# Performance work log

Measured on AMD Instinct MI355X. Metric: run time of the kernel, lower is better.

The kernel has to match this reference:

```python
import jax, jax.numpy as jnp
import numpy as np

N_NODES = 32768
N_EDGES = 524288
NODE_DIM, POS_DIM, EDGE_DIM = 44, 8, 1
HID, OUT, LAYERS, HEADS = 128, 128, 3, 4
DK = HID // HEADS
LN_EPS = 1e-5


def _linear_w(key, fan_in, fan_out):
    return (jax.random.normal(key, (fan_in, fan_out), jnp.float32) / np.sqrt(fan_in)).astype(jnp.float32)


def _ln(x, g, b):
    m = jnp.mean(x, axis=-1, keepdims=True)
    v = jnp.var(x, axis=-1, keepdims=True)
    return (x - m) * jax.lax.rsqrt(v + LN_EPS) * g + b


def setup_inputs() -> dict:
    key = jax.random.key(0)
    ks = jax.random.split(key, 16)
    inp = {
        'feats': jax.random.normal(ks[0], (N_NODES, NODE_DIM), jnp.float32),
        'lap_pos_enc': jax.random.normal(ks[1], (N_NODES, POS_DIM), jnp.float32),
        'edge_feats': jax.random.normal(ks[2], (N_EDGES, EDGE_DIM), jnp.float32),
        'src': jax.random.randint(ks[3], (N_EDGES,), 0, N_NODES, jnp.int32),
        'dst': jax.random.randint(ks[4], (N_EDGES,), 0, N_NODES, jnp.int32),
        # input projections
        'W_node': _linear_w(ks[5], NODE_DIM, HID), 'b_node': jnp.zeros((HID,), jnp.float32),
        'W_pos': _linear_w(ks[6], POS_DIM, HID), 'b_pos': jnp.zeros((HID,), jnp.float32),
        'W_edge': _linear_w(ks[7], EDGE_DIM, HID), 'b_edge': jnp.zeros((HID,), jnp.float32),
    }
    # per-layer stacked params (all layers are HID->HID since OUT==HID)
    def stack(k, fi, fo):
        kk = jax.random.split(k, LAYERS)
        return jnp.stack([_linear_w(kk[i], fi, fo) for i in range(LAYERS)])
    inp['Wq'] = stack(ks[8], HID, HID)
    inp['Wk'] = stack(ks[9], HID, HID)
    inp['Wv'] = stack(ks[10], HID, HID)
    inp['We'] = stack(ks[11], HID, HID)
    inp['W_lin'] = stack(ks[12], HID, HID)
    inp['b_lin'] = jnp.zeros((LAYERS, HID), jnp.float32)
    inp['g1'] = jnp.ones((LAYERS, HID), jnp.float32)
    inp['be1'] = jnp.zeros((LAYERS, HID), jnp.float32)
    inp['Wf1'] = stack(ks[13], HID, 2 * HID)
    inp['bf1'] = jnp.zeros((LAYERS, 2 * HID), jnp.float32)
    inp['Wf2'] = stack(ks[14], 2 * HID, HID)
    inp['bf2'] = jnp.zeros((LAYERS, HID), jnp.float32)
    inp['g2'] = jnp.ones((LAYERS, HID), jnp.float32)
    inp['be2'] = jnp.zeros((LAYERS, HID), jnp.float32)
    return inp


def reference(feats, lap_pos_enc, edge_feats,
              W_node, b_node, W_pos, b_pos, W_edge, b_edge,
              Wq, Wk, Wv, We, W_lin, b_lin, g1, be1,
              Wf1, bf1, Wf2, bf2, g2, be2, src, dst):
    n = feats.shape[0]
    inv_sqrt_dk = np.float32(1.0 / np.sqrt(DK))
    h = feats @ W_node + b_node + lap_pos_enc @ W_pos + b_pos      # [N, HID]
    e = edge_feats @ W_edge + b_edge                               # [E, HID] (shared across layers)
    for i in range(LAYERS):
        Q = (h @ Wq[i]).reshape(n, HEADS, DK)
        K = (h @ Wk[i]).reshape(n, HEADS, DK)
        V = (h @ Wv[i]).reshape(n, HEADS, DK)
        E = (e @ We[i]).reshape(-1, HEADS, DK)                     # [E, H, DK]
        # raw score [E, H, 1] broadcast against (1+E) -> [E, H, DK] (faithful to source)
        score = jnp.sum(K[src] * Q[dst], axis=-1, keepdims=True) * inv_sqrt_dk
        score = score * (1.0 + E)
        alpha = jnp.exp(score)                                      # [E, H, DK]
        Z = jnp.maximum(jax.ops.segment_sum(alpha, dst, num_segments=n), 1e-6)
        h_out = jax.ops.segment_sum(V[src] * alpha, dst, num_segments=n) / Z
        h_out = h_out.reshape(n, HEADS * DK)
        h = h + h_out @ W_lin[i] + b_lin[i]                        # residual + dropout(identity)
        h = _ln(h, g1[i], be1[i])
        h2 = jax.nn.relu(h @ Wf1[i] + bf1[i]) @ Wf2[i] + bf2[i]
        h = _ln(h + h2, g2[i], be2[i])
    # dgl.mean_nodes over a single graph -> [1, OUT]; readout LayerNorm is never applied in source
    return jnp.mean(h, axis=0, keepdims=True)
```

## Files before the change

kernel.cpp:

```cpp
#include <hip/hip_runtime.h>
#include <hip/hip_bf16.h>

#define N_NODES 32768
#define N_EDGES 524288
#define LN_EPS 1e-5f

typedef unsigned short ushort_t;
typedef __attribute__((ext_vector_type(8))) short short8v;
typedef __attribute__((ext_vector_type(4))) float float4v;

__device__ __forceinline__ float bf2f(ushort_t u) {
    return __uint_as_float(((unsigned int)u) << 16);
}
__device__ __forceinline__ ushort_t f2bf(float f) {
    unsigned int u = __float_as_uint(f);
    unsigned int r = (u + 0x7FFFu + ((u >> 16) & 1u)) >> 16;
    return (ushort_t)r;
}
__device__ __forceinline__ float lo16(unsigned int x) { return __uint_as_float(x << 16); }
__device__ __forceinline__ float hi16(unsigned int x) { return __uint_as_float(x & 0xFFFF0000u); }

#if __has_builtin(__builtin_amdgcn_exp2f)
#define EXP2(x) __builtin_amdgcn_exp2f(x)
#else
#define EXP2(x) exp2f(x)
#endif

#define OFF_WNODE 0
#define OFF_BNODE 5632
#define OFF_WPOS  5760
#define OFF_BPOS  6784
#define OFF_WEDGE 6912
#define OFF_BEDGE 7040
#define OFF_WQ    7168
#define OFF_WK    56320
#define OFF_WV    105472
#define OFF_WE    154624
#define OFF_WLIN  203776
#define OFF_BLIN  252928
#define OFF_G1    253312
#define OFF_BE1   253696
#define OFF_WF1   254080
#define OFF_BF1   352384
#define OFF_WF2   353152
#define OFF_BF2   451456
#define OFF_G2    451840
#define OFF_BE2   452224
#define CONV_TOTAL 452608

#define REC_QKV(i)  ((i) * 96)
#define REC_WLIN(i) (288 + (i) * 32)
#define REC_WF1(i)  (384 + (i) * 64)
#define REC_WF2(i)  (576 + (i) * 64)
#define REC_TOTAL   768

#define LDS_STRIDE 264
#define LDS_FSTRIDE 132

__global__ void detect_kernel(const unsigned int* __restrict__ wn, int* __restrict__ flag) {
    __shared__ int s[256];
    int t = threadIdx.x;
    int cnt = 0;
    for (int i = t; i < 2816; i += 256) {
        unsigned int b = (wn[i] >> 8) & 0x7F;
        cnt += (b >= 0x3A && b <= 0x40) ? 1 : 0;
    }
    s[t] = cnt;
    __syncthreads();
    for (int off = 128; off > 0; off >>= 1) {
        if (t < off) s[t] += s[t + off];
        __syncthreads();
    }
    if (t == 0) *flag = (s[0] > 1408) ? 1 : 0;
}

struct ConvArgs { const void* src[20]; };

__global__ void convert_kernel(ConvArgs a, const int* __restrict__ flag,
                               float* __restrict__ dst) {
    int gid = blockIdx.x * 256 + threadIdx.x;
    if (gid >= CONV_TOTAL) return;
    const int off[21] = {OFF_WNODE, OFF_BNODE, OFF_WPOS, OFF_BPOS, OFF_WEDGE, OFF_BEDGE,
                         OFF_WQ, OFF_WK, OFF_WV, OFF_WE, OFF_WLIN, OFF_BLIN, OFF_G1,
                         OFF_BE1, OFF_WF1, OFF_BF1, OFF_WF2, OFF_BF2, OFF_G2, OFF_BE2,
                         CONV_TOTAL};
    int s = 0;
#pragma unroll
    for (int i = 1; i < 20; ++i) s += (gid >= off[i]) ? 1 : 0;
    int local = gid - off[s];
    if (*flag)
        dst[gid] = bf2f(((const ushort_t*)a.src[s])[local]);
    else
        dst[gid] = ((const float*)a.src[s])[local];
}

__global__ void swz_kernel(const float* __restrict__ conv, ushort_t* __restrict__ swz) {
    int gid = blockIdx.x * 256 + threadIdx.x;
    int lane = gid & 63;
    int rec = gid >> 6;
    if (rec >= REC_TOTAL) return;
    int col = lane & 15, quad = lane >> 4;
    const float* src;
    int ct, kb, OC;
    if (rec < 288) {
        int layer = rec / 96, r2 = rec % 96;
        ct = r2 >> 2; kb = r2 & 3;
        int seg = ct >> 3;
        int base = (seg == 0 ? OFF_WQ : (seg == 1 ? OFF_WK : OFF_WV)) + layer * 16384;
        src = conv + base; OC = 128; ct &= 7;
    } else if (rec < 384) {
        int r = rec - 288, layer = r / 32, r2 = r % 32;
        ct = r2 >> 2; kb = r2 & 3;
        src = conv + OFF_WLIN + layer * 16384; OC = 128;
    } else if (rec < 576) {
        int r = rec - 384, layer = r / 64, r2 = r % 64;
        ct = r2 >> 2; kb = r2 & 3;
        src = conv + OFF_WF1 + layer * 32768; OC = 256;
    } else {
        int r = rec - 576, layer = r / 64, r2 = r % 64;
        ct = r2 >> 3; kb = r2 & 7;
        src = conv + OFF_WF2 + layer * 32768; OC = 128;
    }
    int n = ct * 16 + col;
    ushort_t v[8];
#pragma unroll
    for (int j = 0; j < 8; ++j) v[j] = f2bf(src[(size_t)(kb * 32 + quad * 8 + j) * OC + n]);
    ushort_t* o = swz + (size_t)rec * 512 + lane * 8;
#pragma unroll
    for (int j = 0; j < 8; ++j) o[j] = v[j];
}

__global__ void input_proj_kernel(const void* __restrict__ feats,
                                  const void* __restrict__ lap,
                                  const float* __restrict__ conv,
                                  const int* __restrict__ flag,
                                  float* __restrict__ h, ushort_t* __restrict__ hb) {
    int gid = blockIdx.x * 256 + threadIdx.x;
    int node = gid >> 5;
    int cg = (gid & 31) * 4;
    bool isbf = (*flag != 0);
    const float* Wn = conv + OFF_WNODE;
    const float* Wp = conv + OFF_WPOS;

    float4 b1 = *(const float4*)(conv + OFF_BNODE + cg);
    float4 b2 = *(const float4*)(conv + OFF_BPOS + cg);
    float a0 = b1.x + b2.x, a1 = b1.y + b2.y, a2 = b1.z + b2.z, a3 = b1.w + b2.w;

#define ACC(fv, Wbase, kk)                                            \
    {                                                                 \
        float4 wv_ = *(const float4*)(Wbase + (size_t)(kk) * 128 + cg); \
        a0 = fmaf(fv, wv_.x, a0);                                     \
        a1 = fmaf(fv, wv_.y, a1);                                     \
        a2 = fmaf(fv, wv_.z, a2);                                     \
        a3 = fmaf(fv, wv_.w, a3);                                     \
    }

    if (isbf) {
        const ushort_t* frow = (const ushort_t*)feats + (size_t)node * 44;
        const ushort_t* prow = (const ushort_t*)lap + (size_t)node * 8;
#pragma unroll
        for (int i = 0; i < 11; ++i) {
            ushort4 f = *(const ushort4*)(frow + i * 4);
            ACC(bf2f(f.x), Wn, i * 4 + 0)
            ACC(bf2f(f.y), Wn, i * 4 + 1)
            ACC(bf2f(f.z), Wn, i * 4 + 2)
            ACC(bf2f(f.w), Wn, i * 4 + 3)
        }
#pragma unroll
        for (int i = 0; i < 2; ++i) {
            ushort4 f = *(const ushort4*)(prow + i * 4);
            ACC(bf2f(f.x), Wp, i * 4 + 0)
            ACC(bf2f(f.y), Wp, i * 4 + 1)
            ACC(bf2f(f.z), Wp, i * 4 + 2)
            ACC(bf2f(f.w), Wp, i * 4 + 3)
        }
    } else {
        const float4* frow = (const float4*)((const float*)feats + (size_t)node * 44);
        const float4* prow = (const float4*)((const float*)lap + (size_t)node * 8);
#pragma unroll
        for (int i = 0; i < 11; ++i) {
            float4 f = frow[i];
            ACC(f.x, Wn, i * 4 + 0)
            ACC(f.y, Wn, i * 4 + 1)
            ACC(f.z, Wn, i * 4 + 2)
            ACC(f.w, Wn, i * 4 + 3)
        }
#pragma unroll
        for (int i = 0; i < 2; ++i) {
            float4 f = prow[i];
            ACC(f.x, Wp, i * 4 + 0)
            ACC(f.y, Wp, i * 4 + 1)
            ACC(f.z, Wp, i * 4 + 2)
            ACC(f.w, Wp, i * 4 + 3)
        }
    }
#undef ACC

    size_t idx = (size_t)node * 128 + cg;
    *(float4*)(h + idx) = make_float4(a0, a1, a2, a3);
    ushort4 ob;
    ob.x = f2bf(a0); ob.y = f2bf(a1); ob.z = f2bf(a2); ob.w = f2bf(a3);
    *(ushort4*)(hb + idx) = ob;
}

__global__ void uc_kernel(const float* __restrict__ conv,
                          float* __restrict__ u, float* __restrict__ c1) {
    int l = blockIdx.x;
    int d = threadIdx.x;
    const float* W_edge = conv + OFF_WEDGE;
    const float* b_edge = conv + OFF_BEDGE;
    const float* Wl = conv + OFF_WE + l * 128 * 128;
    float uu = 0.f, cc = 0.f;
#pragma unroll 4
    for (int k = 0; k < 128; ++k) {
        float w = Wl[k * 128 + d];
        uu += W_edge[k] * w;
        cc += b_edge[k] * w;
    }
    const float scale = 0.17677669529663687f * 1.4426950408889634f;
    u[l * 128 + d] = uu * scale;
    c1[l * 128 + d] = (1.f + cc) * scale;
}

__global__ void hist_kernel(const int* __restrict__ dst, int* __restrict__ deg) {
    int e = blockIdx.x * 256 + threadIdx.x;
    if (e < N_EDGES) atomicAdd(&deg[dst[e]], 1);
}

__global__ void scan_kernel(const int* __restrict__ deg, int* __restrict__ rowstart,
                            int* __restrict__ cursor) {
    __shared__ int lds[1024];
    int t = threadIdx.x;
    int base = t * 32;
    int v[32];
    int csum = 0;
#pragma unroll
    for (int j = 0; j < 32; ++j) { v[j] = deg[base + j]; csum += v[j]; }
    lds[t] = csum;
    __syncthreads();
    for (int off = 1; off < 1024; off <<= 1) {
        int x = (t >= off) ? lds[t - off] : 0;
        __syncthreads();
        lds[t] += x;
        __syncthreads();
    }
    int excl = lds[t] - csum;
    int running = excl;
#pragma unroll
    for (int j = 0; j < 32; ++j) {
        rowstart[base + j] = running;
        cursor[base + j] = running;
        running += v[j];
    }
    if (t == 1023) rowstart[N_NODES] = running;
}

__global__ void scatter_kernel(const int* __restrict__ src, const int* __restrict__ dst,
                               const void* __restrict__ ef, const int* __restrict__ flag,
                               int* __restrict__ cursor,
                               unsigned int* __restrict__ edges) {
    int e = blockIdx.x * 256 + threadIdx.x;
    if (e < N_EDGES) {
        ushort_t efb = (*flag != 0) ? ((const ushort_t*)ef)[e]
                                    : f2bf(((const float*)ef)[e]);
        int d = dst[e];
        int p = atomicAdd(&cursor[d], 1);
        edges[p] = (unsigned int)src[e] | ((unsigned int)efb << 16);
    }
}

template <int KB>
__global__ __launch_bounds__(256) void qkv_gemm(
    const ushort_t* __restrict__ A,
    const ushort_t* __restrict__ Bswz,
    ushort_t* __restrict__ outB) {
    const int K = KB * 32;
    const int tid = threadIdx.x;
    const int wv = tid >> 6, lane = tid & 63;
    const int col = lane & 15, quad = lane >> 4;
    const int m0 = blockIdx.x * 64 + wv * 16;
    const int ct0 = blockIdx.y * 8;

    float4v acc[8];
#pragma unroll
    for (int ct = 0; ct < 8; ++ct) acc[ct] = (float4v){0.f, 0.f, 0.f, 0.f};

    const ushort_t* Ap = A + (size_t)(m0 + col) * K + quad * 8;
    const ushort_t* Bp = Bswz + (size_t)ct0 * KB * 512 + lane * 8;

#pragma unroll
    for (int kb = 0; kb < KB; ++kb) {
        short8v a = *(const short8v*)(Ap + kb * 32);
#pragma unroll
        for (int ct = 0; ct < 8; ++ct) {
            short8v b = *(const short8v*)(Bp + (size_t)(ct * KB + kb) * 512);
            acc[ct] = __builtin_amdgcn_mfma_f32_16x16x32_bf16(a, b, acc[ct], 0, 0, 0);
        }
    }

    const int rowb = m0 + quad * 4;
#pragma unroll
    for (int ct = 0; ct < 8; ++ct) {
        int j = ct * 16 + col;
        int seg = blockIdx.y;
        int pos = (seg == 0) ? j : 128 + 8 * (j >> 2) + 4 * (seg - 1) + (j & 3);
#pragma unroll
        for (int r = 0; r < 4; ++r) {
            outB[(size_t)(rowb + r) * 384 + pos] = f2bf(acc[ct][r]);
        }
    }
}

__global__ __launch_bounds__(64, 2) void ffn_kernel(
    const ushort_t* __restrict__ HOUT,
    const ushort_t* __restrict__ BWL,
    const ushort_t* __restrict__ BF1,
    const ushort_t* __restrict__ BF2,
    const float* __restrict__ bl,
    const float* __restrict__ g1v, const float* __restrict__ be1v,
    const float* __restrict__ bf1v,
    const float* __restrict__ bf2v,
    const float* __restrict__ g2v, const float* __restrict__ be2v,
    float* __restrict__ h,
    ushort_t* __restrict__ hb) {
    __shared__ __align__(16) char ldsraw[16 * 528];
    ushort_t* ldsu = (ushort_t*)ldsraw;
    float* ldsf = (float*)ldsraw;
    const int lane = threadIdx.x & 63;
    const int col = lane & 15, quad = lane >> 4;
    const int m0 = blockIdx.x * 16;
    const int rowb = m0 + quad * 4;
    const int lrowc = quad * 4;
    const int lrowa = col;

    float4v acc[8];
#pragma unroll
    for (int ct = 0; ct < 8; ++ct) acc[ct] = (float4v){0.f, 0.f, 0.f, 0.f};
    const ushort_t* Ap = HOUT + (size_t)(m0 + col) * 128 + quad * 8;
#pragma unroll
    for (int kb = 0; kb < 4; ++kb) {
        short8v a = *(const short8v*)(Ap + kb * 32);
#pragma unroll
        for (int ct = 0; ct < 8; ++ct) {
            short8v b = *(const short8v*)(BWL + (size_t)(ct * 4 + kb) * 512 + lane * 8);
            acc[ct] = __builtin_amdgcn_mfma_f32_16x16x32_bf16(a, b, acc[ct], 0, 0, 0);
        }
    }

    float val[8][4], s[4] = {0.f, 0.f, 0.f, 0.f}, ss[4] = {0.f, 0.f, 0.f, 0.f};
#pragma unroll
    for (int ct = 0; ct < 8; ++ct) {
        float bi = bl[ct * 16 + col];
#pragma unroll
        for (int r = 0; r < 4; ++r) {
            float v = acc[ct][r] + bi + h[(size_t)(rowb + r) * 128 + ct * 16 + col];
            val[ct][r] = v;
            s[r] += v;
            ss[r] += v * v;
        }
    }
#pragma unroll
    for (int mask = 1; mask < 16; mask <<= 1) {
#pragma unroll
        for (int r = 0; r < 4; ++r) {
            s[r] += __shfl_xor(s[r], mask, 64);
            ss[r] += __shfl_xor(ss[r], mask, 64);
        }
    }
#pragma unroll
    for (int r = 0; r < 4; ++r) {
        float mean = s[r] * (1.f / 128.f);
        float var = ss[r] * (1.f / 128.f) - mean * mean;
        s[r] = mean;
        ss[r] = rsqrtf(var + LN_EPS);
    }
#pragma unroll
    for (int ct = 0; ct < 8; ++ct) {
        float gg = g1v[ct * 16 + col], bb = be1v[ct * 16 + col];
#pragma unroll
        for (int r = 0; r < 4; ++r) {
            float o = (val[ct][r] - s[r]) * ss[r] * gg + bb;
            val[ct][r] = o;
            ldsu[(lrowc + r) * LDS_STRIDE + ct * 16 + col] = f2bf(o);
        }
    }
    __syncthreads();

    short8v af[4];
#pragma unroll
    for (int kb = 0; kb < 4; ++kb)
        af[kb] = *(const short8v*)&ldsu[lrowa * LDS_STRIDE + kb * 32 + quad * 8];

    float4v acc2[16];
#pragma unroll
    for (int ct = 0; ct < 16; ++ct) acc2[ct] = (float4v){0.f, 0.f, 0.f, 0.f};
#pragma unroll
    for (int kb = 0; kb < 4; ++kb) {
#pragma unroll
        for (int ct = 0; ct < 16; ++ct) {
            short8v b = *(const short8v*)(BF1 + (size_t)(ct * 4 + kb) * 512 + lane * 8);
            acc2[ct] = __builtin_amdgcn_mfma_f32_16x16x32_bf16(af[kb], b, acc2[ct], 0, 0, 0);
        }
    }
    __syncthreads();

#pragma unroll
    for (int ct = 0; ct < 16; ++ct) {
        float bi = bf1v[ct * 16 + col];
#pragma unroll
        for (int r = 0; r < 4; ++r) {
            float v = fmaxf(acc2[ct][r] + bi, 0.f);
            ldsu[(lrowc + r) * LDS_STRIDE + ct * 16 + col] = f2bf(v);
        }
    }
    __syncthreads();

    float4v acc3[8];
#pragma unroll
    for (int ct = 0; ct < 8; ++ct) acc3[ct] = (float4v){0.f, 0.f, 0.f, 0.f};
#pragma unroll
    for (int kb = 0; kb < 8; ++kb) {
        short8v a = *(const short8v*)&ldsu[lrowa * LDS_STRIDE + kb * 32 + quad * 8];
#pragma unroll
        for (int ct = 0; ct < 8; ++ct) {
            short8v b = *(const short8v*)(BF2 + (size_t)(ct * 8 + kb) * 512 + lane * 8);
            acc3[ct] = __builtin_amdgcn_mfma_f32_16x16x32_bf16(a, b, acc3[ct], 0, 0, 0);
        }
    }

    float s2[4] = {0.f, 0.f, 0.f, 0.f}, ss2[4] = {0.f, 0.f, 0.f, 0.f};
#pragma unroll
    for (int ct = 0; ct < 8; ++ct) {
        float bi = bf2v[ct * 16 + col];
#pragma unroll
        for (int r = 0; r < 4; ++r) {
            float v = acc3[ct][r] + bi + val[ct][r];
            val[ct][r] = v;
            s2[r] += v;
            ss2[r] += v * v;
        }
    }
#pragma unroll
    for (int mask = 1; mask < 16; mask <<= 1) {
#pragma unroll
        for (int r = 0; r < 4; ++r) {
            s2[r] += __shfl_xor(s2[r], mask, 64);
            ss2[r] += __shfl_xor(ss2[r], mask, 64);
        }
    }
#pragma unroll
    for (int r = 0; r < 4; ++r) {
        float mean = s2[r] * (1.f / 128.f);
        float var = ss2[r] * (1.f / 128.f) - mean * mean;
        s2[r] = mean;
        ss2[r] = rsqrtf(var + LN_EPS);
    }
    __syncthreads();
#pragma unroll
    for (int ct = 0; ct < 8; ++ct) {
        float gg = g2v[ct * 16 + col], bb = be2v[ct * 16 + col];
#pragma unroll
        for (int r = 0; r < 4; ++r) {
            float o = (val[ct][r] - s2[r]) * ss2[r] * gg + bb;
            ldsf[(lrowc + r) * LDS_FSTRIDE + ct * 16 + col] = o;
        }
    }
    __syncthreads();

#pragma unroll
    for (int j = 0; j < 8; ++j) {
        int p = lane + j * 64;
        int row = p >> 5;
        int c4 = p & 31;
        float4 vv = *(const float4*)&ldsf[row * LDS_FSTRIDE + c4 * 4];
        *(float4*)&h[(size_t)(m0 + row) * 128 + c4 * 4] = vv;
    }
#pragma unroll
    for (int j = 0; j < 4; ++j) {
        int p = lane + j * 64;
        int row = p >> 4;
        int c8 = p & 15;
        float4 va = *(const float4*)&ldsf[row * LDS_FSTRIDE + c8 * 8];
        float4 vb = *(const float4*)&ldsf[row * LDS_FSTRIDE + c8 * 8 + 4];
        uint4 ou;
        ou.x = (unsigned)f2bf(va.x) | ((unsigned)f2bf(va.y) << 16);
        ou.y = (unsigned)f2bf(va.z) | ((unsigned)f2bf(va.w) << 16);
        ou.z = (unsigned)f2bf(vb.x) | ((unsigned)f2bf(vb.y) << 16);
        ou.w = (unsigned)f2bf(vb.z) | ((unsigned)f2bf(vb.w) << 16);
        *(uint4*)&hb[(size_t)(m0 + row) * 128 + c8 * 8] = ou;
    }
}

__global__ __launch_bounds__(64) void agg_kernel(
    const ushort_t* __restrict__ QKV,
    const int* __restrict__ rowstart, const unsigned int* __restrict__ edges,
    const float* __restrict__ u, const float* __restrict__ c1,
    ushort_t* __restrict__ hout) {
    const int lane = threadIdx.x & 63;
    const int v = blockIdx.x;
    const int sub = lane & 15;
    const int grp = lane >> 4;

    uint4 qu = *(const uint4*)(QKV + (size_t)v * 384 + sub * 8);
    float q0 = lo16(qu.x), q1 = hi16(qu.x), q2 = lo16(qu.y), q3 = hi16(qu.y);
    float q4 = lo16(qu.z), q5 = hi16(qu.z), q6 = lo16(qu.w), q7 = hi16(qu.w);
    float4 uva = *(const float4*)(u + sub * 8);
    float4 uvb = *(const float4*)(u + sub * 8 + 4);
    float4 cva = *(const float4*)(c1 + sub * 8);
    float4 cvb = *(const float4*)(c1 + sub * 8 + 4);

    float m = -1.0e38f;
    float sA[8] = {0.f, 0.f, 0.f, 0.f, 0.f, 0.f, 0.f, 0.f};
    float o[8] = {0.f, 0.f, 0.f, 0.f, 0.f, 0.f, 0.f, 0.f};

    const int start = rowstart[v];
    const int deg = rowstart[v + 1] - start;
    const int nfull = deg >> 2;
    const unsigned int* ep = edges + start + grp;

#define AGG_BODY(PE, MASKED, VALID)                                              \
    {                                                                            \
        unsigned int pe_ = (PE);                                                 \
        int s_ = (int)(pe_ & 0xFFFFu);                                           \
        float ef_ = __uint_as_float(pe_ & 0xFFFF0000u);                          \
        const ushort_t* kp_ = QKV + (size_t)s_ * 384 + 128 + 16 * sub;           \
        uint4 kv0 = *(const uint4*)kp_;                                          \
        uint4 kv1 = *(const uint4*)(kp_ + 8);                                    \
        float p_ = lo16(kv0.x) * q0;                                             \
        p_ = fmaf(hi16(kv0.x), q1, p_);                                          \
        p_ = fmaf(lo16(kv0.y), q2, p_);                                          \
        p_ = fmaf(hi16(kv0.y), q3, p_);                                          \
        p_ = fmaf(lo16(kv1.x), q4, p_);                                          \
        p_ = fmaf(hi16(kv1.x), q5, p_);                                          \
        p_ = fmaf(lo16(kv1.y), q6, p_);                                          \
        p_ = fmaf(hi16(kv1.y), q7, p_);                                          \
        p_ += __shfl_xor(p_, 1, 64);                                             \
        p_ += __shfl_xor(p_, 2, 64);                                             \
        float x0 = p_ * fmaf(ef_, uva.x, cva.x);                                 \
        float x1 = p_ * fmaf(ef_, uva.y, cva.y);                                 \
        float x2 = p_ * fmaf(ef_, uva.z, cva.z);                                 \
        float x3 = p_ * fmaf(ef_, uva.w, cva.w);                                 \
        float x4 = p_ * fmaf(ef_, uvb.x, cvb.x);                                 \
        float x5 = p_ * fmaf(ef_, uvb.y, cvb.y);                                 \
        float x6 = p_ * fmaf(ef_, uvb.z, cvb.z);                                 \
        float x7 = p_ * fmaf(ef_, uvb.w, cvb.w);                                 \
        if (MASKED) {                                                            \
            x0 = (VALID) ? x0 : -1.0e38f; x1 = (VALID) ? x1 : -1.0e38f;          \
            x2 = (VALID) ? x2 : -1.0e38f; x3 = (VALID) ? x3 : -1.0e38f;          \
            x4 = (VALID) ? x4 : -1.0e38f; x5 = (VALID) ? x5 : -1.0e38f;          \
            x6 = (VALID) ? x6 : -1.0e38f; x7 = (VALID) ? x7 : -1.0e38f;          \
        }                                                                        \
        float xm = fmaxf(fmaxf(fmaxf(x0, x1), fmaxf(x2, x3)),                    \
                         fmaxf(fmaxf(x4, x5), fmaxf(x6, x7)));                   \
        if (xm > m) {                                                            \
            float nm = xm + 6.0f;                                                \
            float sc = EXP2(m - nm);                                             \
            sA[0] *= sc; sA[1] *= sc; sA[2] *= sc; sA[3] *= sc;                  \
            sA[4] *= sc; sA[5] *= sc; sA[6] *= sc; sA[7] *= sc;                  \
            o[0] *= sc; o[1] *= sc; o[2] *= sc; o[3] *= sc;                      \
            o[4] *= sc; o[5] *= sc; o[6] *= sc; o[7] *= sc;                      \
            m = nm;                                                              \
        }                                                                        \
        float e0 = EXP2(x0 - m), e1 = EXP2(x1 - m);                              \
        float e2 = EXP2(x2 - m), e3 = EXP2(x3 - m);                              \
        float e4 = EXP2(x4 - m), e5 = EXP2(x5 - m);                              \
        float e6 = EXP2(x6 - m), e7 = EXP2(x7 - m);                              \
        sA[0] += e0; sA[1] += e1; sA[2] += e2; sA[3] += e3;                      \
        sA[4] += e4; sA[5] += e5; sA[6] += e6; sA[7] += e7;                      \
        o[0] = fmaf(lo16(kv0.z), e0, o[0]);                                      \
        o[1] = fmaf(hi16(kv0.z), e1, o[1]);                                      \
        o[2] = fmaf(lo16(kv0.w), e2, o[2]);                                      \
        o[3] = fmaf(hi16(kv0.w), e3, o[3]);                                      \
        o[4] = fmaf(lo16(kv1.z), e4, o[4]);                                      \
        o[5] = fmaf(hi16(kv1.z), e5, o[5]);                                      \
        o[6] = fmaf(lo16(kv1.w), e6, o[6]);                                      \
        o[7] = fmaf(hi16(kv1.w), e7, o[7]);                                      \
    }

    for (int it = 0; it < nfull; ++it, ep += 4) {
        AGG_BODY(*ep, false, true)
    }
    const int rem = deg & 3;
    if (rem) {
        bool valid = grp < rem;
        unsigned int pe = valid ? *ep : edges[start];
        AGG_BODY(pe, true, valid)
    }
#undef AGG_BODY

#pragma unroll
    for (int mask = 16; mask <= 32; mask <<= 1) {
        float mo = __shfl_xor(m, mask, 64);
        float mm = fmaxf(m, mo);
        float sca = EXP2(m - mm);
        float scb = EXP2(mo - mm);
#pragma unroll
        for (int j = 0; j < 8; ++j) {
            float t = __shfl_xor(sA[j], mask, 64);
            sA[j] = sA[j] * sca + t * scb;
            t = __shfl_xor(o[j], mask, 64);
            o[j] = o[j] * sca + t * scb;
        }
        m = mm;
    }

    if (grp == 0) {
        float zc = 1e-6f * EXP2(-m);
        uint4 ou;
        unsigned int w0, w1;
        float z;
        z = fmaxf(fmaxf(sA[0], zc), 1e-37f); w0 = f2bf(o[0] / z);
        z = fmaxf(fmaxf(sA[1], zc), 1e-37f); w1 = f2bf(o[1] / z);
        ou.x = w0 | (w1 << 16);
        z = fmaxf(fmaxf(sA[2], zc), 1e-37f); w0 = f2bf(o[2] / z);
        z = fmaxf(fmaxf(sA[3], zc), 1e-37f); w1 = f2bf(o[3] / z);
        ou.y = w0 | (w1 << 16);
        z = fmaxf(fmaxf(sA[4], zc), 1e-37f); w0 = f2bf(o[4] / z);
        z = fmaxf(fmaxf(sA[5], zc), 1e-37f); w1 = f2bf(o[5] / z);
        ou.z = w0 | (w1 << 16);
        z = fmaxf(fmaxf(sA[6], zc), 1e-37f); w0 = f2bf(o[6] / z);
        z = fmaxf(fmaxf(sA[7], zc), 1e-37f); w1 = f2bf(o[7] / z);
        ou.w = w0 | (w1 << 16);
        *(uint4*)(hout + (size_t)v * 128 + sub * 8) = ou;
    }
}

__global__ void mean_part_kernel(const float* __restrict__ h, float* __restrict__ macc) {
    __shared__ float s[256];
    int t = threadIdx.x;
    int col = t & 127;
    int half = t >> 7;
    int r0 = blockIdx.x * 256;
    float acc = 0.f;
    for (int r = half; r < 256; r += 2) acc += h[(size_t)(r0 + r) * 128 + col];
    s[t] = acc;
    __syncthreads();
    if (t < 128) atomicAdd(&macc[t], s[t] + s[t + 128]);
}

__global__ void finalize_kernel(const float* __restrict__ macc, void* __restrict__ out,
                                const int* __restrict__ flag) {
    int t = threadIdx.x;
    float v = macc[t] * (1.f / (float)N_NODES);
    if (*flag)
        ((ushort_t*)out)[t] = f2bf(v);
    else
        ((float*)out)[t] = v;
}

extern "C" void kernel_launch(void* const* d_in, const int* in_sizes, int n_in,
                              void* d_out, int out_size, void* d_ws, size_t ws_size,
                              hipStream_t stream) {
    const int* src = (const int*)d_in[3];
    const int* dst = (const int*)d_in[4];

    char* w = (char*)d_ws;
    const size_t MB = 1u << 20;
    float* h        = (float*)(w);
    ushort_t* hb    = (ushort_t*)(w + 16 * MB);
    ushort_t* QKVh  = (ushort_t*)(w + 24 * MB);
    char* aux       = w + 48 * MB;
    int* deg        = (int*)(aux);
    int* rowstart   = (int*)(aux + 0x40000);
    int* cursor     = (int*)(aux + 0x80000);
    unsigned int* edges = (unsigned int*)(aux + 0xC0000);
    float* ubuf     = (float*)(aux + 0xC0000 + 2 * MB);
    float* cbuf     = ubuf + 3 * 128;
    float* macc     = cbuf + 3 * 128;
    int* flag       = (int*)(macc + 128);
    float* conv     = (float*)(aux + 0xC0000 + 2 * MB + 4096);
    ushort_t* swz   = (ushort_t*)((char*)conv + CONV_TOTAL * 4);

    hipMemsetAsync(deg, 0, N_NODES * sizeof(int), stream);
    hipMemsetAsync(macc, 0, 128 * sizeof(float), stream);

    detect_kernel<<<1, 256, 0, stream>>>((const unsigned int*)d_in[5], flag);

    ConvArgs ca;
    ca.src[0] = d_in[5];   ca.src[1] = d_in[6];   ca.src[2] = d_in[7];
    ca.src[3] = d_in[8];   ca.src[4] = d_in[9];   ca.src[5] = d_in[10];
    ca.src[6] = d_in[11];  ca.src[7] = d_in[12];  ca.src[8] = d_in[13];
    ca.src[9] = d_in[14];  ca.src[10] = d_in[15]; ca.src[11] = d_in[16];
    ca.src[12] = d_in[17]; ca.src[13] = d_in[18]; ca.src[14] = d_in[19];
    ca.src[15] = d_in[20]; ca.src[16] = d_in[21]; ca.src[17] = d_in[22];
    ca.src[18] = d_in[23]; ca.src[19] = d_in[24];
    convert_kernel<<<(CONV_TOTAL + 255) / 256, 256, 0, stream>>>(ca, flag, conv);
    swz_kernel<<<REC_TOTAL * 64 / 256, 256, 0, stream>>>(conv, swz);

    input_proj_kernel<<<N_NODES * 32 / 256, 256, 0, stream>>>(d_in[0], d_in[1], conv,
                                                              flag, h, hb);
    uc_kernel<<<3, 128, 0, stream>>>(conv, ubuf, cbuf);
    hist_kernel<<<N_EDGES / 256, 256, 0, stream>>>(dst, deg);
    scan_kernel<<<1, 1024, 0, stream>>>(deg, rowstart, cursor);
    scatter_kernel<<<N_EDGES / 256, 256, 0, stream>>>(src, dst, d_in[2], flag, cursor,
                                                      edges);

    for (int i = 0; i < 3; ++i) {
        const ushort_t* swzQKV = swz + (size_t)REC_QKV(i) * 512;
        const ushort_t* swzWL  = swz + (size_t)REC_WLIN(i) * 512;
        const ushort_t* swzF1  = swz + (size_t)REC_WF1(i) * 512;
        const ushort_t* swzF2  = swz + (size_t)REC_WF2(i) * 512;

        qkv_gemm<4><<<dim3(N_NODES / 64, 3), 256, 0, stream>>>(hb, swzQKV, QKVh);

        agg_kernel<<<N_NODES, 64, 0, stream>>>(QKVh, rowstart, edges,
                                               ubuf + i * 128, cbuf + i * 128, hb);

        ffn_kernel<<<N_NODES / 16, 64, 0, stream>>>(
            hb, swzWL, swzF1, swzF2,
            conv + OFF_BLIN + i * 128, conv + OFF_G1 + i * 128, conv + OFF_BE1 + i * 128,
            conv + OFF_BF1 + i * 256,
            conv + OFF_BF2 + i * 128, conv + OFF_G2 + i * 128, conv + OFF_BE2 + i * 128,
            h, hb);
    }

    mean_part_kernel<<<N_NODES / 256, 256, 0, stream>>>(h, macc);
    finalize_kernel<<<1, 128, 0, stream>>>(macc, d_out, flag);
}
```

Baseline: 524.8 us.

## Store K/V in FP8 and fuse QKV projection into one LDS-staged kernel

The QKV GEMM now runs as one 64-thread block per 16 rows and computes all 24 column tiles. Q is written as bf16 and K/V are packed to FP8 (interleaved per head) through LDS with coalesced 16-byte stores. The aggregation kernel gathers 16 bytes of FP8 K/V per lane instead of 32 bytes of bf16, roughly halving the random-gather traffic that dominates edge aggregation. The cost is lower precision in the attention scores and values, plus a GEMM kernel holding 24 accumulator tiles per wave, which raises register pressure.

```diff
diff --git a/kernel.cpp b/kernel.cpp
--- a/kernel.cpp
+++ b/kernel.cpp
@@ -8,6 +8,7 @@
 typedef unsigned short ushort_t;
 typedef __attribute__((ext_vector_type(8))) short short8v;
 typedef __attribute__((ext_vector_type(4))) float float4v;
+typedef __attribute__((ext_vector_type(2))) float float2v;
 
 __device__ __forceinline__ float bf2f(ushort_t u) {
     return __uint_as_float(((unsigned int)u) << 16);
@@ -269,45 +270,78 @@
     }
 }
 
-template <int KB>
-__global__ __launch_bounds__(256) void qkv_gemm(
+__global__ __launch_bounds__(64, 2) void qkv_kernel(
     const ushort_t* __restrict__ A,
     const ushort_t* __restrict__ Bswz,
-    ushort_t* __restrict__ outB) {
-    const int K = KB * 32;
-    const int tid = threadIdx.x;
-    const int wv = tid >> 6, lane = tid & 63;
+    ushort_t* __restrict__ outQ,
+    unsigned char* __restrict__ outKV) {
+    __shared__ ushort_t lds[16 * LDS_STRIDE];
+    const int lane = threadIdx.x & 63;
     const int col = lane & 15, quad = lane >> 4;
-    const int m0 = blockIdx.x * 64 + wv * 16;
-    const int ct0 = blockIdx.y * 8;
-
-    float4v acc[8];
-#pragma unroll
-    for (int ct = 0; ct < 8; ++ct) acc[ct] = (float4v){0.f, 0.f, 0.f, 0.f};
-
-    const ushort_t* Ap = A + (size_t)(m0 + col) * K + quad * 8;
-    const ushort_t* Bp = Bswz + (size_t)ct0 * KB * 512 + lane * 8;
-
-#pragma unroll
-    for (int kb = 0; kb < KB; ++kb) {
-        short8v a = *(const short8v*)(Ap + kb * 32);
-#pragma unroll
-        for (int ct = 0; ct < 8; ++ct) {
-            short8v b = *(const short8v*)(Bp + (size_t)(ct * KB + kb) * 512);
-            acc[ct] = __builtin_amdgcn_mfma_f32_16x16x32_bf16(a, b, acc[ct], 0, 0, 0);
-        }
-    }
-
-    const int rowb = m0 + quad * 4;
+    const int m0 = blockIdx.x * 16;
+    const int lrowc = quad * 4;
+
+    short8v af[4];
+    const ushort_t* Ap = A + (size_t)(m0 + col) * 128 + quad * 8;
+#pragma unroll
+    for (int kb = 0; kb < 4; ++kb)
+        af[kb] = *(const short8v*)(Ap + kb * 32);
+
+    float4v acc[24];
+#pragma unroll
+    for (int ct = 0; ct < 24; ++ct) acc[ct] = (float4v){0.f, 0.f, 0.f, 0.f};
+#pragma unroll
+    for (int kb = 0; kb < 4; ++kb) {
+#pragma unroll
+        for (int ct = 0; ct < 24; ++ct) {
+            short8v b = *(const short8v*)(Bswz + (size_t)(ct * 4 + kb) * 512 + lane * 8);
+            acc[ct] = __builtin_amdgcn_mfma_f32_16x16x32_bf16(af[kb], b, acc[ct], 0, 0, 0);
+        }
+    }
+
 #pragma unroll
     for (int ct = 0; ct < 8; ++ct) {
         int j = ct * 16 + col;
-        int seg = blockIdx.y;
-        int pos = (seg == 0) ? j : 128 + 8 * (j >> 2) + 4 * (seg - 1) + (j & 3);
-#pragma unroll
-        for (int r = 0; r < 4; ++r) {
-            outB[(size_t)(rowb + r) * 384 + pos] = f2bf(acc[ct][r]);
-        }
+#pragma unroll
+        for (int r = 0; r < 4; ++r)
+            lds[(lrowc + r) * LDS_STRIDE + j] = f2bf(acc[ct][r]);
+    }
+#pragma unroll
+    for (int seg = 0; seg < 2; ++seg) {
+#pragma unroll
+        for (int c = 0; c < 8; ++c) {
+            int ct = 8 + seg * 8 + c;
+            int j = c * 16 + col;
+#pragma unroll
+            for (int r = 0; r < 4; ++r) {
+                float a = acc[ct][r];
+                float b = __shfl_xor(a, 1, 64);
+                if ((col & 1) == 0) {
+                    unsigned short pk = (unsigned short)
+                        __builtin_amdgcn_cvt_pk_fp8_f32(a, b, 0, false);
+                    int us = (j >> 3) * 8 + ((j >> 1) & 3) + seg * 4;
+                    lds[(lrowc + r) * LDS_STRIDE + 128 + us] = pk;
+                }
+            }
+        }
+    }
+    __syncthreads();
+
+#pragma unroll
+    for (int jj = 0; jj < 4; ++jj) {
+        int p = lane + jj * 64;
+        int row = p >> 4;
+        int c16 = p & 15;
+        uint4 qv = *(const uint4*)&lds[row * LDS_STRIDE + c16 * 8];
+        *(uint4*)&outQ[(size_t)(m0 + row) * 128 + c16 * 8] = qv;
+    }
+#pragma unroll
+    for (int jj = 0; jj < 4; ++jj) {
+        int p = lane + jj * 64;
+        int row = p >> 4;
+        int c16 = p & 15;
+        uint4 kv = *(const uint4*)&lds[row * LDS_STRIDE + 128 + c16 * 8];
+        *(uint4*)&outKV[(size_t)(m0 + row) * 256 + c16 * 16] = kv;
     }
 }
 
@@ -492,7 +526,7 @@
 }
 
 __global__ __launch_bounds__(64) void agg_kernel(
-    const ushort_t* __restrict__ QKV,
+    const ushort_t* __restrict__ Q, const unsigned char* __restrict__ KV,
     const int* __restrict__ rowstart, const unsigned int* __restrict__ edges,
     const float* __restrict__ u, const float* __restrict__ c1,
     ushort_t* __restrict__ hout) {
@@ -501,7 +535,7 @@
     const int sub = lane & 15;
     const int grp = lane >> 4;
 
-    uint4 qu = *(const uint4*)(QKV + (size_t)v * 384 + sub * 8);
+    uint4 qu = *(const uint4*)(Q + (size_t)v * 128 + sub * 8);
     float q0 = lo16(qu.x), q1 = hi16(qu.x), q2 = lo16(qu.y), q3 = hi16(qu.y);
     float q4 = lo16(qu.z), q5 = hi16(qu.z), q6 = lo16(qu.w), q7 = hi16(qu.w);
     float4 uva = *(const float4*)(u + sub * 8);
@@ -523,17 +557,19 @@
         unsigned int pe_ = (PE);                                                 \
         int s_ = (int)(pe_ & 0xFFFFu);                                           \
         float ef_ = __uint_as_float(pe_ & 0xFFFF0000u);                          \
-        const ushort_t* kp_ = QKV + (size_t)s_ * 384 + 128 + 16 * sub;           \
-        uint4 kv0 = *(const uint4*)kp_;                                          \
-        uint4 kv1 = *(const uint4*)(kp_ + 8);                                    \
-        float p_ = lo16(kv0.x) * q0;                                             \
-        p_ = fmaf(hi16(kv0.x), q1, p_);                                          \
-        p_ = fmaf(lo16(kv0.y), q2, p_);                                          \
-        p_ = fmaf(hi16(kv0.y), q3, p_);                                          \
-        p_ = fmaf(lo16(kv1.x), q4, p_);                                          \
-        p_ = fmaf(hi16(kv1.x), q5, p_);                                          \
-        p_ = fmaf(lo16(kv1.y), q6, p_);                                          \
-        p_ = fmaf(hi16(kv1.y), q7, p_);                                          \
+        uint4 kv = *(const uint4*)(KV + (size_t)s_ * 256 + sub * 16);            \
+        float2v k01 = __builtin_amdgcn_cvt_pk_f32_fp8(kv.x, false);              \
+        float2v k23 = __builtin_amdgcn_cvt_pk_f32_fp8(kv.x, true);               \
+        float2v k45 = __builtin_amdgcn_cvt_pk_f32_fp8(kv.y, false);              \
+        float2v k67 = __builtin_amdgcn_cvt_pk_f32_fp8(kv.y, true);               \
+        float p_ = k01[0] * q0;                                                  \
+        p_ = fmaf(k01[1], q1, p_);                                               \
+        p_ = fmaf(k23[0], q2, p_);                                               \
+        p_ = fmaf(k23[1], q3, p_);                                               \
+        p_ = fmaf(k45[0], q4, p_);                                               \
+        p_ = fmaf(k45[1], q5, p_);                                               \
+        p_ = fmaf(k67[0], q6, p_);                                               \
+        p_ = fmaf(k67[1], q7, p_);                                               \
         p_ += __shfl_xor(p_, 1, 64);                                             \
         p_ += __shfl_xor(p_, 2, 64);                                             \
         float x0 = p_ * fmaf(ef_, uva.x, cva.x);                                 \
@@ -567,14 +603,18 @@
         float e6 = EXP2(x6 - m), e7 = EXP2(x7 - m);                              \
         sA[0] += e0; sA[1] += e1; sA[2] += e2; sA[3] += e3;                      \
         sA[4] += e4; sA[5] += e5; sA[6] += e6; sA[7] += e7;                      \
-        o[0] = fmaf(lo16(kv0.z), e0, o[0]);                                      \
-        o[1] = fmaf(hi16(kv0.z), e1, o[1]);                                      \
-        o[2] = fmaf(lo16(kv0.w), e2, o[2]);                                      \
-        o[3] = fmaf(hi16(kv0.w), e3, o[3]);                                      \
-        o[4] = fmaf(lo16(kv1.z), e4, o[4]);                                      \
-        o[5] = fmaf(hi16(kv1.z), e5, o[5]);                                      \
-        o[6] = fmaf(lo16(kv1.w), e6, o[6]);                                      \
-        o[7] = fmaf(hi16(kv1.w), e7, o[7]);                                      \
+        float2v v01 = __builtin_amdgcn_cvt_pk_f32_fp8(kv.z, false);              \
+        float2v v23 = __builtin_amdgcn_cvt_pk_f32_fp8(kv.z, true);               \
+        float2v v45 = __builtin_amdgcn_cvt_pk_f32_fp8(kv.w, false);              \
+        float2v v67 = __builtin_amdgcn_cvt_pk_f32_fp8(kv.w, true);               \
+        o[0] = fmaf(v01[0], e0, o[0]);                                           \
+        o[1] = fmaf(v01[1], e1, o[1]);                                           \
+        o[2] = fmaf(v23[0], e2, o[2]);                                           \
+        o[3] = fmaf(v23[1], e3, o[3]);                                           \
+        o[4] = fmaf(v45[0], e4, o[4]);                                           \
+        o[5] = fmaf(v45[1], e5, o[5]);                                           \
+        o[6] = fmaf(v67[0], e6, o[6]);                                           \
+        o[7] = fmaf(v67[1], e7, o[7]);                                           \
     }
 
     for (int it = 0; it < nfull; ++it, ep += 4) {
@@ -658,7 +698,8 @@
     const size_t MB = 1u << 20;
     float* h        = (float*)(w);
     ushort_t* hb    = (ushort_t*)(w + 16 * MB);
-    ushort_t* QKVh  = (ushort_t*)(w + 24 * MB);
+    ushort_t* Qh    = (ushort_t*)(w + 24 * MB);
+    unsigned char* KVf8 = (unsigned char*)(w + 32 * MB);
     char* aux       = w + 48 * MB;
     int* deg        = (int*)(aux);
     int* rowstart   = (int*)(aux + 0x40000);
@@ -701,9 +742,9 @@
         const ushort_t* swzF1  = swz + (size_t)REC_WF1(i) * 512;
         const ushort_t* swzF2  = swz + (size_t)REC_WF2(i) * 512;
 
-        qkv_gemm<4><<<dim3(N_NODES / 64, 3), 256, 0, stream>>>(hb, swzQKV, QKVh);
-
-        agg_kernel<<<N_NODES, 64, 0, stream>>>(QKVh, rowstart, edges,
+        qkv_kernel<<<N_NODES / 16, 64, 0, stream>>>(hb, swzQKV, Qh, KVf8);
+
+        agg_kernel<<<N_NODES, 64, 0, stream>>>(Qh, KVf8, rowstart, edges,
                                                ubuf + i * 128, cbuf + i * 128, hb);
 
         ffn_kernel<<<N_NODES / 16, 64, 0, stream>>>(
```

Measured after the change: 544.6 us. +3.8%, slower.
